# Performance work log

Measured on AMD Instinct MI355X. Metric: run time of the kernel, lower is better.

Reference implementation:

```python
import jax, jax.numpy as jnp
import numpy as np

N_NODES = 100000


def _gcn_layer(x, src, dst, ew, norm_s, norm_d, W, b):
    # DGL GraphConv with edge weights, norm='both':
    # h_v = D_in(v)^-1/2 * sum_{(u,v) in E} w_uv * D_out(u)^-1/2 * x_u; then Linear.
    m = (x * norm_s[:, None])[src] * ew[:, None]        # [E, d] gather + weight
    agg = jax.ops.segment_sum(m, dst, num_segments=N_NODES)  # [N, d] scatter-add
    return (agg * norm_d[:, None]) @ W + b


def setup_inputs() -> dict:
    key = jax.random.key(0)
    ks = jax.random.split(key, 12)
    N, E, D, C = N_NODES, 1600000, 64, 32
    inp = {
        "x": jax.random.normal(ks[0], (N, D), jnp.float32),
        "src": jax.random.randint(ks[1], (E,), 0, N, jnp.int64),
        "dst": jax.random.randint(ks[2], (E,), 0, N, jnp.int64),
        "ew": jax.random.uniform(ks[3], (E,), jnp.float32),
    }
    s = 1.0 / np.sqrt(D)
    for i, k in zip(range(1, 5), ks[4:8]):
        inp[f"W{i}"] = jax.random.normal(k, (D, D), jnp.float32) * s
        inp[f"b{i}"] = jnp.zeros((D,), jnp.float32)
    inp["Wr"] = jax.random.normal(ks[8], (D, D), jnp.float32) * s
    inp["br"] = jnp.zeros((D,), jnp.float32)
    inp["Wo"] = jax.random.normal(ks[9], (D, C), jnp.float32) * s
    inp["bo"] = jnp.zeros((C,), jnp.float32)
    return inp


def reference(x, src, dst, ew, W1, b1, W2, b2, W3, b3, W4, b4, Wr, br, Wo, bo):
    ones = jnp.ones(src.shape, x.dtype)
    deg_out = jnp.clip(jax.ops.segment_sum(ones, src, num_segments=N_NODES), 1.0)
    deg_in = jnp.clip(jax.ops.segment_sum(ones, dst, num_segments=N_NODES), 1.0)
    norm_s = deg_out ** -0.5
    norm_d = deg_in ** -0.5

    res = x @ Wr + br
    h = jax.nn.relu(_gcn_layer(x, src, dst, ew, norm_s, norm_d, W1, b1))
    h = jax.nn.relu(_gcn_layer(h, src, dst, ew, norm_s, norm_d, W2, b2))
    h = jax.nn.relu(_gcn_layer(h, src, dst, ew, norm_s, norm_d, W3, b3))
    h = _gcn_layer(h, src, dst, ew, norm_s, norm_d, W4, b4)
    h = jax.nn.relu(h + res)
    return h @ Wo + bo
```

## Files before the change

### kernel.cpp

```cpp
#include <hip/hip_runtime.h>

#define NN 100000
#define D 64
#define G 3
#define RS 33334
#define NC 85
#define NB (G*NC)

typedef short bf16x8 __attribute__((ext_vector_type(8)));
typedef float f32x4 __attribute__((ext_vector_type(4)));
typedef float f32x2 __attribute__((ext_vector_type(2)));

__device__ __forceinline__ float bf2f_lo(unsigned w) { return __uint_as_float(w << 16); }
__device__ __forceinline__ float bf2f_hi(unsigned w) { return __uint_as_float(w & 0xffff0000u); }
__device__ __forceinline__ unsigned short f2bf(float f) {
    unsigned u = __float_as_uint(f);
    return (unsigned short)((u + 0x7fffu + ((u >> 16) & 1u)) >> 16);
}
__device__ __forceinline__ unsigned pack2(float a, float b) {
    return (unsigned)f2bf(a) | ((unsigned)f2bf(b) << 16);
}
__device__ __forceinline__ unsigned char f2fp8(float v) {
    return (unsigned char)(__builtin_amdgcn_cvt_pk_fp8_f32(v, v, 0, false) & 0xff);
}
__device__ __forceinline__ unsigned pack_cw(int s, float w) {
    return ((unsigned)f2bf(w) << 17) | (unsigned)s;
}
#define PKFMA(acc, w2, p) \
    asm("v_pk_fma_f32 %0, %1, %2, %0" : "+v"(acc) : "v"(w2), "v"(p))

__global__ __launch_bounds__(1024) void k_hist(const int* __restrict__ src,
                                               const int* __restrict__ dst,
                                               unsigned short* __restrict__ psd, int E) {
    __shared__ unsigned h[RS / 2];
    int b = blockIdx.x, t = threadIdx.x;
    int g = b / NC, c = b - g * NC;
    int lo = g * RS;
    for (int i = t; i < RS / 2; i += 1024) h[i] = 0;
    __syncthreads();
    int e0 = (int)((((long long)c * E / NC)) & ~3LL);
    int e1 = (c == NC - 1) ? E : (int)((((long long)(c + 1) * E / NC)) & ~3LL);
    int m = (e1 - e0) & ~4095;
    for (int e = e0 + t * 4; e < e0 + m; e += 4096) {
        int4 s4 = *(const int4*)(src + e);
        int4 d4 = *(const int4*)(dst + e);
        int v;
        v = s4.x - lo; if ((unsigned)v < RS) atomicAdd(&h[v >> 1], 1u << ((v & 1) * 16));
        v = s4.y - lo; if ((unsigned)v < RS) atomicAdd(&h[v >> 1], 1u << ((v & 1) * 16));
        v = s4.z - lo; if ((unsigned)v < RS) atomicAdd(&h[v >> 1], 1u << ((v & 1) * 16));
        v = s4.w - lo; if ((unsigned)v < RS) atomicAdd(&h[v >> 1], 1u << ((v & 1) * 16));
        v = d4.x - lo; if ((unsigned)v < RS) atomicAdd(&h[v >> 1], 1u << ((v & 1) * 16 + 8));
        v = d4.y - lo; if ((unsigned)v < RS) atomicAdd(&h[v >> 1], 1u << ((v & 1) * 16 + 8));
        v = d4.z - lo; if ((unsigned)v < RS) atomicAdd(&h[v >> 1], 1u << ((v & 1) * 16 + 8));
        v = d4.w - lo; if ((unsigned)v < RS) atomicAdd(&h[v >> 1], 1u << ((v & 1) * 16 + 8));
    }
    for (int e = e0 + m + t; e < e1; e += 1024) {
        int v = src[e] - lo; if ((unsigned)v < RS) atomicAdd(&h[v >> 1], 1u << ((v & 1) * 16));
        v = dst[e] - lo;     if ((unsigned)v < RS) atomicAdd(&h[v >> 1], 1u << ((v & 1) * 16 + 8));
    }
    __syncthreads();
    unsigned* pb = (unsigned*)(psd + (size_t)b * RS);
    for (int i = t; i < RS / 2; i += 1024) pb[i] = h[i];
}

__global__ __launch_bounds__(1024) void k_scan1m(const unsigned short* __restrict__ psd,
                                                 float* __restrict__ ns, float* __restrict__ nd,
                                                 int* __restrict__ rowptr,
                                                 int* __restrict__ bsum, int n) {
    __shared__ int lds[1024];
    int t = threadIdx.x;
    int i = blockIdx.x * 1024 + t;
    int sv = 0, dv = 0;
    if (i < n) {
        int g = i / RS, off = i - g * RS;
        const unsigned short* p = psd + (size_t)(g * NC) * RS + off;
        #pragma unroll 5
        for (int c = 0; c < NC; ++c) {
            unsigned v = p[(size_t)c * RS];
            sv += (int)(v & 0xffu);
            dv += (int)(v >> 8);
        }
        ns[i] = rsqrtf(fmaxf((float)sv, 1.0f));
        nd[i] = rsqrtf(fmaxf((float)dv, 1.0f));
    }
    lds[t] = dv;
    __syncthreads();
    for (int off = 1; off < 1024; off <<= 1) {
        int v = lds[t];
        int a = (t >= off) ? lds[t - off] : 0;
        __syncthreads();
        lds[t] = v + a;
        __syncthreads();
    }
    if (t == 1023) bsum[blockIdx.x] = lds[1023];
    if (i < n) rowptr[i] = lds[t] - dv;
}

__global__ void k_scan3c(int* __restrict__ rowptr, const int* __restrict__ bsum,
                         const unsigned short* __restrict__ psd,
                         unsigned short* __restrict__ cur16,
                         int n, int E, int nb) {
    __shared__ int sbs[128];
    int t = threadIdx.x;
    if (t < 128) sbs[t] = (t < nb) ? bsum[t] : 0;
    __syncthreads();
    for (int off = 1; off < 128; off <<= 1) {
        int v = 0, a = 0;
        if (t < 128) { v = sbs[t]; if (t >= off) a = sbs[t - off]; }
        __syncthreads();
        if (t < 128) sbs[t] = v + a;
        __syncthreads();
    }
    int i = blockIdx.x * blockDim.x + t;
    if (i == 0) rowptr[n] = E;
    if (i >= n) return;
    int blk = i >> 10;
    int base = (blk > 0) ? sbs[blk - 1] : 0;
    int r = rowptr[i] + base;
    rowptr[i] = r;
    int g = i / RS, off = i - g * RS;
    const unsigned short* p = psd + (size_t)(g * NC) * RS + off;
    unsigned short* cp = cur16 + (size_t)(g * NC) * RS + off;
    int run = 0;
    #pragma unroll 5
    for (int c = 0; c < NC; ++c) {
        cp[(size_t)c * RS] = (unsigned short)run;
        run += (int)(p[(size_t)c * RS] >> 8);
    }
}

__global__ __launch_bounds__(1024) void k_fillsort(const int* __restrict__ src,
                                                   const int* __restrict__ dst,
                                                   const float* __restrict__ ew,
                                                   const int* __restrict__ rowptr,
                                                   const unsigned short* __restrict__ cur16,
                                                   unsigned* __restrict__ cw, int E) {
    __shared__ int cur[RS];
    int b = blockIdx.x, t = threadIdx.x;
    int g = b / NC, c = b - g * NC;
    int lo = g * RS;
    const unsigned short* c16 = cur16 + (size_t)b * RS;
    for (int i = t; i < RS; i += 1024) cur[i] = rowptr[lo + i] + (int)c16[i];
    __syncthreads();
    int e0 = (int)((((long long)c * E / NC)) & ~3LL);
    int e1 = (c == NC - 1) ? E : (int)((((long long)(c + 1) * E / NC)) & ~3LL);
    int m = (e1 - e0) & ~4095;
    for (int e = e0 + t * 4; e < e0 + m; e += 4096) {
        int4 s4 = *(const int4*)(src + e);
        int4 d4 = *(const int4*)(dst + e);
        float4 w4 = *(const float4*)(ew + e);
        int d;
        d = d4.x - lo; if ((unsigned)d < RS) { int p = atomicAdd(&cur[d], 1); cw[p] = pack_cw(s4.x, w4.x); }
        d = d4.y - lo; if ((unsigned)d < RS) { int p = atomicAdd(&cur[d], 1); cw[p] = pack_cw(s4.y, w4.y); }
        d = d4.z - lo; if ((unsigned)d < RS) { int p = atomicAdd(&cur[d], 1); cw[p] = pack_cw(s4.z, w4.z); }
        d = d4.w - lo; if ((unsigned)d < RS) { int p = atomicAdd(&cur[d], 1); cw[p] = pack_cw(s4.w, w4.w); }
    }
    for (int e = e0 + m + t; e < e1; e += 1024) {
        int d = dst[e] - lo;
        if ((unsigned)d < RS) {
            int p = atomicAdd(&cur[d], 1);
            cw[p] = pack_cw(src[e], ew[e]);
        }
    }
}

__global__ __launch_bounds__(256) void k_gemm2(const float* __restrict__ x,
                                               const float* __restrict__ Wr,
                                               const float* __restrict__ brs,
                                               const float* __restrict__ W1,
                                               const float* __restrict__ ns,
                                               unsigned short* __restrict__ resb,
                                               unsigned char* __restrict__ tmat, int n) {
    __shared__ unsigned short WTr[64][72];
    __shared__ unsigned short WT1[64][72];
    int t = threadIdx.x;
    for (int i = t; i < 64 * 64; i += 256) {
        int k = i >> 6, nn = i & 63;
        WTr[nn][k] = f2bf(Wr[i]);
        WT1[nn][k] = f2bf(W1[i]);
    }
    __syncthreads();
    int w = t >> 6, lane = t & 63;
    int m = lane & 15, q = lane >> 4;
    int node0 = blockIdx.x * 64 + w * 16;
    int nodeA = min(node0 + m, n - 1);
    const float* inf = x + (size_t)nodeA * D;
    float sc = ns[nodeA];
    bf16x8 afr[2], afs[2];
    #pragma unroll
    for (int kc = 0; kc < 2; ++kc) {
        float4 f0 = *(const float4*)(inf + kc * 32 + q * 8);
        float4 f1 = *(const float4*)(inf + kc * 32 + q * 8 + 4);
        union { bf16x8 v; unsigned short u[8]; } ta, ts;
        ta.u[0] = f2bf(f0.x); ta.u[1] = f2bf(f0.y);
        ta.u[2] = f2bf(f0.z); ta.u[3] = f2bf(f0.w);
        ta.u[4] = f2bf(f1.x); ta.u[5] = f2bf(f1.y);
        ta.u[6] = f2bf(f1.z); ta.u[7] = f2bf(f1.w);
        ts.u[0] = f2bf(f0.x * sc); ts.u[1] = f2bf(f0.y * sc);
        ts.u[2] = f2bf(f0.z * sc); ts.u[3] = f2bf(f0.w * sc);
        ts.u[4] = f2bf(f1.x * sc); ts.u[5] = f2bf(f1.y * sc);
        ts.u[6] = f2bf(f1.z * sc); ts.u[7] = f2bf(f1.w * sc);
        afr[kc] = ta.v;
        afs[kc] = ts.v;
    }
    #pragma unroll
    for (int nt = 0; nt < 4; ++nt) {
        f32x4 ar = {0.f, 0.f, 0.f, 0.f};
        f32x4 at = {0.f, 0.f, 0.f, 0.f};
        #pragma unroll
        for (int kc = 0; kc < 2; ++kc) {
            union { bf16x8 v; uint4 u; } bfr, bf1;
            bfr.u = *(const uint4*)&WTr[nt * 16 + m][kc * 32 + q * 8];
            bf1.u = *(const uint4*)&WT1[nt * 16 + m][kc * 32 + q * 8];
            ar = __builtin_amdgcn_mfma_f32_16x16x32_bf16(afr[kc], bfr.v, ar, 0, 0, 0);
            at = __builtin_amdgcn_mfma_f32_16x16x32_bf16(afs[kc], bf1.v, at, 0, 0, 0);
        }
        int col = nt * 16 + m;
        float bb = brs[col];
        #pragma unroll
        for (int r = 0; r < 4; ++r) {
            int node = node0 + q * 4 + r;
            if (node < n) {
                resb[(size_t)node * D + col] = f2bf(ar[r] + bb);
                tmat[(size_t)node * D + col] = f2fp8(at[r]);
            }
        }
    }
}

template<bool LAST>
__global__ void k_gather(const int* __restrict__ rowptr, const unsigned* __restrict__ cw,
                         const unsigned char* __restrict__ tmat,
                         const float* __restrict__ nd, const float* __restrict__ ns,
                         const float* __restrict__ bias,
                         const unsigned short* __restrict__ resb,
                         unsigned short* __restrict__ outb, int n, int E) {
    int grp = threadIdx.x >> 3;
    int h   = threadIdx.x & 7;
    int node = blockIdx.x * 32 + grp;
    bool valid = node < n;
    int nc = valid ? node : 0;
    int beg = rowptr[nc];
    int end = valid ? rowptr[nc + 1] : beg;
    unsigned h8 = (unsigned)(h * 8);
    f32x2 A0={0.f,0.f},A1={0.f,0.f},A2={0.f,0.f},A3={0.f,0.f};
    f32x2 C0={0.f,0.f},C1={0.f,0.f},C2={0.f,0.f},C3={0.f,0.f};
    unsigned cvA = (beg     < end) ? cw[beg]     : 0u;
    unsigned cvB = (beg + 1 < end) ? cw[beg + 1] : 0u;
    unsigned cvC = (beg + 2 < end) ? cw[beg + 2] : 0u;
    unsigned cvD = (beg + 3 < end) ? cw[beg + 3] : 0u;
    for (int e = beg; e < end; e += 4) {
        uint2 rA = *(const uint2*)(tmat + (((cvA & 0x1FFFFu) << 6) + h8));
        uint2 rB = *(const uint2*)(tmat + (((cvB & 0x1FFFFu) << 6) + h8));
        uint2 rC = *(const uint2*)(tmat + (((cvC & 0x1FFFFu) << 6) + h8));
        uint2 rD = *(const uint2*)(tmat + (((cvD & 0x1FFFFu) << 6) + h8));
        int f = e + 4;
        unsigned nvA = (f     < end) ? cw[f]     : 0u;
        unsigned nvB = (f + 1 < end) ? cw[f + 1] : 0u;
        unsigned nvC = (f + 2 < end) ? cw[f + 2] : 0u;
        unsigned nvD = (f + 3 < end) ? cw[f + 3] : 0u;
        float wA = __uint_as_float((cvA >> 17) << 16);
        float wB = __uint_as_float((cvB >> 17) << 16);
        float wC = __uint_as_float((cvC >> 17) << 16);
        float wD = __uint_as_float((cvD >> 17) << 16);
        f32x2 w2A = {wA, wA}, w2B = {wB, wB}, w2C = {wC, wC}, w2D = {wD, wD};
        f32x2 p;
        p = __builtin_amdgcn_cvt_pk_f32_fp8(rA.x, false); PKFMA(A0, w2A, p);
        p = __builtin_amdgcn_cvt_pk_f32_fp8(rA.x, true);  PKFMA(A1, w2A, p);
        p = __builtin_amdgcn_cvt_pk_f32_fp8(rA.y, false); PKFMA(A2, w2A, p);
        p = __builtin_amdgcn_cvt_pk_f32_fp8(rA.y, true);  PKFMA(A3, w2A, p);
        p = __builtin_amdgcn_cvt_pk_f32_fp8(rB.x, false); PKFMA(C0, w2B, p);
        p = __builtin_amdgcn_cvt_pk_f32_fp8(rB.x, true);  PKFMA(C1, w2B, p);
        p = __builtin_amdgcn_cvt_pk_f32_fp8(rB.y, false); PKFMA(C2, w2B, p);
        p = __builtin_amdgcn_cvt_pk_f32_fp8(rB.y, true);  PKFMA(C3, w2B, p);
        p = __builtin_amdgcn_cvt_pk_f32_fp8(rC.x, false); PKFMA(A0, w2C, p);
        p = __builtin_amdgcn_cvt_pk_f32_fp8(rC.x, true);  PKFMA(A1, w2C, p);
        p = __builtin_amdgcn_cvt_pk_f32_fp8(rC.y, false); PKFMA(A2, w2C, p);
        p = __builtin_amdgcn_cvt_pk_f32_fp8(rC.y, true);  PKFMA(A3, w2C, p);
        p = __builtin_amdgcn_cvt_pk_f32_fp8(rD.x, false); PKFMA(C0, w2D, p);
        p = __builtin_amdgcn_cvt_pk_f32_fp8(rD.x, true);  PKFMA(C1, w2D, p);
        p = __builtin_amdgcn_cvt_pk_f32_fp8(rD.y, false); PKFMA(C2, w2D, p);
        p = __builtin_amdgcn_cvt_pk_f32_fp8(rD.y, true);  PKFMA(C3, w2D, p);
        cvA = nvA; cvB = nvB; cvC = nvC; cvD = nvD;
    }
    if (!valid) return;
    float a0 = A0.x + C0.x, a1 = A0.y + C0.y;
    float a2 = A1.x + C1.x, a3 = A1.y + C1.y;
    float a4 = A2.x + C2.x, a5 = A2.y + C2.y;
    float a6 = A3.x + C3.x, a7 = A3.y + C3.y;
    float ndv = nd[node];
    float4 b0 = *(const float4*)(bias + 8 * h);
    float4 b1 = *(const float4*)(bias + 8 * h + 4);
    float v0 = ndv * a0 + b0.x, v1 = ndv * a1 + b0.y;
    float v2 = ndv * a2 + b0.z, v3 = ndv * a3 + b0.w;
    float v4 = ndv * a4 + b1.x, v5 = ndv * a5 + b1.y;
    float v6 = ndv * a6 + b1.z, v7 = ndv * a7 + b1.w;
    if (LAST) {
        uint4 r = *((const uint4*)(resb + (size_t)node * D) + h);
        v0 += bf2f_lo(r.x); v1 += bf2f_hi(r.x);
        v2 += bf2f_lo(r.y); v3 += bf2f_hi(r.y);
        v4 += bf2f_lo(r.z); v5 += bf2f_hi(r.z);
        v6 += bf2f_lo(r.w); v7 += bf2f_hi(r.w);
    }
    v0 = fmaxf(v0, 0.f); v1 = fmaxf(v1, 0.f); v2 = fmaxf(v2, 0.f); v3 = fmaxf(v3, 0.f);
    v4 = fmaxf(v4, 0.f); v5 = fmaxf(v5, 0.f); v6 = fmaxf(v6, 0.f); v7 = fmaxf(v7, 0.f);
    if (!LAST) {
        float s = ns[node];
        v0 *= s; v1 *= s; v2 *= s; v3 *= s; v4 *= s; v5 *= s; v6 *= s; v7 *= s;
    }
    uint4 o = make_uint4(pack2(v0, v1), pack2(v2, v3), pack2(v4, v5), pack2(v6, v7));
    *((uint4*)(outb + (size_t)node * D) + h) = o;
}

template<int OUTD, bool BIAS, int OUTMODE>
__global__ __launch_bounds__(256) void k_gemm(const unsigned short* __restrict__ inb,
                                              const float* __restrict__ W,
                                              const float* __restrict__ bias,
                                              void* __restrict__ out_, int n) {
    constexpr int NT = OUTD / 16;
    __shared__ unsigned short WT[OUTD][72];
    int t = threadIdx.x;
    for (int i = t; i < 64 * OUTD; i += 256) {
        int k = i / OUTD, nn = i % OUTD;
        WT[nn][k] = f2bf(W[i]);
    }
    __syncthreads();
    int w = t >> 6, lane = t & 63;
    int m = lane & 15, q = lane >> 4;
    int node0 = blockIdx.x * 64 + w * 16;
    int nodeA = min(node0 + m, n - 1);
    const unsigned short* ip = inb + (size_t)nodeA * D;
    bf16x8 afr[2];
    #pragma unroll
    for (int kc = 0; kc < 2; ++kc) {
        union { bf16x8 v; uint4 u; } tmp;
        tmp.u = *(const uint4*)(ip + kc * 32 + q * 8);
        afr[kc] = tmp.v;
    }
    #pragma unroll
    for (int nt = 0; nt < NT; ++nt) {
        f32x4 acc = {0.f, 0.f, 0.f, 0.f};
        #pragma unroll
        for (int kc = 0; kc < 2; ++kc) {
            union { bf16x8 v; uint4 u; } bfr;
            bfr.u = *(const uint4*)&WT[nt * 16 + m][kc * 32 + q * 8];
            acc = __builtin_amdgcn_mfma_f32_16x16x32_bf16(afr[kc], bfr.v, acc, 0, 0, 0);
        }
        int col = nt * 16 + m;
        float bb = BIAS ? bias[col] : 0.f;
        #pragma unroll
        for (int r = 0; r < 4; ++r) {
            int node = node0 + q * 4 + r;
            if (node < n) {
                float v = acc[r] + bb;
                if (OUTMODE == 2)
                    ((unsigned char*)out_)[(size_t)node * OUTD + col] = f2fp8(v);
                else
                    ((float*)out_)[(size_t)node * OUTD + col] = v;
            }
        }
    }
}

static inline char* align_up(char* p, size_t a) {
    return (char*)(((uintptr_t)p + a - 1) & ~(uintptr_t)(a - 1));
}

extern "C" void kernel_launch(void* const* d_in, const int* in_sizes, int n_in,
                              void* d_out, int out_size, void* d_ws, size_t ws_size,
                              hipStream_t stream) {
    const float* x   = (const float*)d_in[0];
    const int*   src = (const int*)d_in[1];
    const int*   dst = (const int*)d_in[2];
    const float* ew  = (const float*)d_in[3];
    const float* Wl[4] = {(const float*)d_in[4], (const float*)d_in[6],
                          (const float*)d_in[8], (const float*)d_in[10]};
    const float* bl[4] = {(const float*)d_in[5], (const float*)d_in[7],
                          (const float*)d_in[9], (const float*)d_in[11]};
    const float* Wr = (const float*)d_in[12];
    const float* br = (const float*)d_in[13];
    const float* Wo = (const float*)d_in[14];
    const float* bo = (const float*)d_in[15];
    float* out = (float*)d_out;

    const int N = NN;
    const int E = in_sizes[1];

    char* p = (char*)d_ws;
    float* norm_s = (float*)p;            p = align_up(p + N * 4, 256);
    float* norm_d = (float*)p;            p = align_up(p + N * 4, 256);
    int*   rowptr = (int*)p;              p = align_up(p + (size_t)(G * RS + 80) * 4, 256);
    int*   bsum   = (int*)p;              p = align_up(p + 128 * 4, 256);
    unsigned* cw  = (unsigned*)p;         p = align_up(p + (size_t)E * 4, 256);
    unsigned short* psd   = (unsigned short*)p; p = align_up(p + (size_t)NB * RS * 2, 256);
    unsigned short* cur16 = (unsigned short*)p; p = align_up(p + (size_t)NB * RS * 2, 256);
    unsigned short* resb  = (unsigned short*)p; p = align_up(p + (size_t)N * D * 2, 256);
    unsigned short* xs   = psd;
    unsigned char*  tmat = (unsigned char*)(xs + (size_t)N * D);

    k_hist<<<NB, 1024, 0, stream>>>(src, dst, psd, E);
    int nb = (N + 1023) / 1024;
    k_scan1m<<<nb, 1024, 0, stream>>>(psd, norm_s, norm_d, rowptr, bsum, N);
    k_scan3c<<<(N + 255) / 256, 256, 0, stream>>>(rowptr, bsum, psd, cur16, N, E, nb);
    k_fillsort<<<NB, 1024, 0, stream>>>(src, dst, ew, rowptr, cur16, cw, E);

    k_gemm2<<<(N + 63) / 64, 256, 0, stream>>>(x, Wr, br, Wl[0], norm_s, resb, tmat, N);

    k_gather<false><<<(N + 31) / 32, 256, 0, stream>>>(
        rowptr, cw, tmat, norm_d, norm_s, bl[0], nullptr, xs, N, E);
    k_gemm<64, false, 2><<<(N + 63) / 64, 256, 0, stream>>>(xs, Wl[1], nullptr, tmat, N);
    k_gather<false><<<(N + 31) / 32, 256, 0, stream>>>(
        rowptr, cw, tmat, norm_d, norm_s, bl[1], nullptr, xs, N, E);
    k_gemm<64, false, 2><<<(N + 63) / 64, 256, 0, stream>>>(xs, Wl[2], nullptr, tmat, N);
    k_gather<false><<<(N + 31) / 32, 256, 0, stream>>>(
        rowptr, cw, tmat, norm_d, norm_s, bl[2], nullptr, xs, N, E);
    k_gemm<64, false, 2><<<(N + 63) / 64, 256, 0, stream>>>(xs, Wl[3], nullptr, tmat, N);
    k_gather<true><<<(N + 31) / 32, 256, 0, stream>>>(
        rowptr, cw, tmat, norm_d, nullptr, bl[3], resb, xs, N, E);
    k_gemm<32, true, 0><<<(N + 63) / 64, 256, 0, stream>>>(xs, Wo, bo, out, N);
}
```

Measured before the change: 310.3 us.

## Bucket nodes by in-degree so gather wavefronts process similar-length rows

Adds three small kernels that histogram node in-degrees into buckets of four-edge iterations, scan the buckets, and scatter node ids into a degree-sorted order array. Each gather kernel now looks up its node through this order, so the 8-lane groups within a wavefront share similar loop trip counts and spend less time idle from divergence. The cost is three extra launches and an indirection per node. Output writes still index by the real node id, but their addresses are no longer contiguous, which may hurt coalescing and locality.

```diff
diff --git a/kernel.cpp b/kernel.cpp
--- a/kernel.cpp
+++ b/kernel.cpp
@@ -6,6 +6,7 @@
 #define RS 33334
 #define NC 85
 #define NB (G*NC)
+#define SB 98
 
 typedef short bf16x8 __attribute__((ext_vector_type(8)));
 typedef float f32x4 __attribute__((ext_vector_type(4)));
@@ -161,6 +162,58 @@
             int p = atomicAdd(&cur[d], 1);
             cw[p] = pack_cw(src[e], ew[e]);
         }
+    }
+}
+
+__global__ __launch_bounds__(1024) void k_dhist(const int* __restrict__ rowptr,
+                                                int* __restrict__ dh, int n) {
+    __shared__ int hb[64];
+    int t = threadIdx.x;
+    if (t < 64) hb[t] = 0;
+    __syncthreads();
+    int i = blockIdx.x * 1024 + t;
+    if (i < n) {
+        int d = rowptr[i + 1] - rowptr[i];
+        int it = min((d + 3) >> 2, 63);
+        atomicAdd(&hb[it], 1);
+    }
+    __syncthreads();
+    if (t < 64) dh[blockIdx.x * 64 + t] = hb[t];
+}
+
+__global__ __launch_bounds__(64) void k_dscan(int* __restrict__ dh) {
+    __shared__ int tot[64];
+    int k = threadIdx.x;
+    int run = 0;
+    for (int b = 0; b < SB; ++b) {
+        int v = dh[b * 64 + k];
+        dh[b * 64 + k] = run;
+        run += v;
+    }
+    tot[k] = run;
+    __syncthreads();
+    int base = 0;
+    for (int j = 0; j < 64; ++j) {
+        if (j == k) break;
+        base += tot[j];
+    }
+    __syncthreads();
+    for (int b = 0; b < SB; ++b) dh[b * 64 + k] += base;
+}
+
+__global__ __launch_bounds__(1024) void k_dscat(const int* __restrict__ rowptr,
+                                                const int* __restrict__ dh,
+                                                int* __restrict__ ord, int n) {
+    __shared__ int cnt[64];
+    int t = threadIdx.x;
+    if (t < 64) cnt[t] = dh[blockIdx.x * 64 + t];
+    __syncthreads();
+    int i = blockIdx.x * 1024 + t;
+    if (i < n) {
+        int d = rowptr[i + 1] - rowptr[i];
+        int it = min((d + 3) >> 2, 63);
+        int pos = atomicAdd(&cnt[it], 1);
+        ord[pos] = i;
     }
 }
 
@@ -234,14 +287,15 @@
                          const float* __restrict__ nd, const float* __restrict__ ns,
                          const float* __restrict__ bias,
                          const unsigned short* __restrict__ resb,
+                         const int* __restrict__ ord,
                          unsigned short* __restrict__ outb, int n, int E) {
     int grp = threadIdx.x >> 3;
     int h   = threadIdx.x & 7;
-    int node = blockIdx.x * 32 + grp;
-    bool valid = node < n;
-    int nc = valid ? node : 0;
-    int beg = rowptr[nc];
-    int end = valid ? rowptr[nc + 1] : beg;
+    int gid = blockIdx.x * 32 + grp;
+    bool valid = gid < n;
+    int node = valid ? ord[gid] : 0;
+    int beg = rowptr[node];
+    int end = valid ? rowptr[node + 1] : beg;
     unsigned h8 = (unsigned)(h * 8);
     f32x2 A0={0.f,0.f},A1={0.f,0.f},A2={0.f,0.f},A3={0.f,0.f};
     f32x2 C0={0.f,0.f},C1={0.f,0.f},C2={0.f,0.f},C3={0.f,0.f};
@@ -391,7 +445,9 @@
     float* norm_d = (float*)p;            p = align_up(p + N * 4, 256);
     int*   rowptr = (int*)p;              p = align_up(p + (size_t)(G * RS + 80) * 4, 256);
     int*   bsum   = (int*)p;              p = align_up(p + 128 * 4, 256);
-    unsigned* cw  = (unsigned*)p;         p = align_up(p + (size_t)E * 4, 256);
+    int*   dh     = (int*)p;              p = align_up(p + (size_t)SB * 64 * 4, 256);
+    int*   ord    = (int*)p;              p = align_up(p + (size_t)N * 4, 256);
+    unsigned* cw  = (unsigned*)p;         p = align_up(p + (size_t)(E + 8) * 4, 256);
     unsigned short* psd   = (unsigned short*)p; p = align_up(p + (size_t)NB * RS * 2, 256);
     unsigned short* cur16 = (unsigned short*)p; p = align_up(p + (size_t)NB * RS * 2, 256);
     unsigned short* resb  = (unsigned short*)p; p = align_up(p + (size_t)N * D * 2, 256);
@@ -404,18 +460,22 @@
     k_scan3c<<<(N + 255) / 256, 256, 0, stream>>>(rowptr, bsum, psd, cur16, N, E, nb);
     k_fillsort<<<NB, 1024, 0, stream>>>(src, dst, ew, rowptr, cur16, cw, E);
 
+    k_dhist<<<nb, 1024, 0, stream>>>(rowptr, dh, N);
+    k_dscan<<<1, 64, 0, stream>>>(dh);
+    k_dscat<<<nb, 1024, 0, stream>>>(rowptr, dh, ord, N);
+
     k_gemm2<<<(N + 63) / 64, 256, 0, stream>>>(x, Wr, br, Wl[0], norm_s, resb, tmat, N);
 
     k_gather<false><<<(N + 31) / 32, 256, 0, stream>>>(
-        rowptr, cw, tmat, norm_d, norm_s, bl[0], nullptr, xs, N, E);
+        rowptr, cw, tmat, norm_d, norm_s, bl[0], nullptr, ord, xs, N, E);
     k_gemm<64, false, 2><<<(N + 63) / 64, 256, 0, stream>>>(xs, Wl[1], nullptr, tmat, N);
     k_gather<false><<<(N + 31) / 32, 256, 0, stream>>>(
-        rowptr, cw, tmat, norm_d, norm_s, bl[1], nullptr, xs, N, E);
+        rowptr, cw, tmat, norm_d, norm_s, bl[1], nullptr, ord, xs, N, E);
     k_gemm<64, false, 2><<<(N + 63) / 64, 256, 0, stream>>>(xs, Wl[2], nullptr, tmat, N);
     k_gather<false><<<(N + 31) / 32, 256, 0, stream>>>(
-        rowptr, cw, tmat, norm_d, norm_s, bl[2], nullptr, xs, N, E);
+        rowptr, cw, tmat, norm_d, norm_s, bl[2], nullptr, ord, xs, N, E);
     k_gemm<64, false, 2><<<(N + 63) / 64, 256, 0, stream>>>(xs, Wl[3], nullptr, tmat, N);
     k_gather<true><<<(N + 31) / 32, 256, 0, stream>>>(
-        rowptr, cw, tmat, norm_d, nullptr, bl[3], resb, xs, N, E);
+        rowptr, cw, tmat, norm_d, nullptr, bl[3], resb, ord, xs, N, E);
     k_gemm<32, true, 0><<<(N + 63) / 64, 256, 0, stream>>>(xs, Wo, bo, out, N);
 }
```

Result: slower. 334.6 us (+7.8%).
